# Performance work log

Hardware: AMD Instinct MI355X
Metric: run time of the kernel (lower is better)

Reference implementation:

```python
import jax, jax.numpy as jnp
import numpy as np

N, E, H = 20000, 640000, 128
EPS_BN = 1e-5
EPS_NORM = 1e-6


def batchnorm(x, gamma, beta):
    # BatchNorm1d in training mode: biased batch stats over dim 0
    mean = x.mean(axis=0)
    var = x.var(axis=0)
    return (x - mean) * jax.lax.rsqrt(var + EPS_BN) * gamma + beta


def setup_inputs() -> dict:
    key = jax.random.key(0)
    ks = jax.random.split(key, 10)
    s = 1.0 / np.sqrt(H)
    s3 = 1.0 / np.sqrt(3 * H)
    return {
        "edge_index": jax.random.randint(ks[0], (2, E), 0, N, dtype=jnp.int64),
        "node_features": jax.random.normal(ks[1], (N, H), dtype=jnp.float32),
        "edge_features": jax.random.normal(ks[2], (E, H), dtype=jnp.float32),
        "Wg": jax.random.uniform(ks[3], (H, 3 * H), jnp.float32, -s3, s3),
        "bg": jax.random.uniform(ks[4], (H,), jnp.float32, -s3, s3),
        "Ws": jax.random.uniform(ks[5], (H, H), jnp.float32, -s, s),
        "bs": jax.random.uniform(ks[6], (H,), jnp.float32, -s, s),
        "Wd": jax.random.uniform(ks[7], (H, H), jnp.float32, -s, s),
        "bd": jax.random.uniform(ks[8], (H,), jnp.float32, -s, s),
        "z_gamma": jnp.ones((H,), jnp.float32),
        "z_beta": jnp.zeros((H,), jnp.float32),
        "n_gamma": jnp.ones((H,), jnp.float32),
        "n_beta": jnp.zeros((H,), jnp.float32),
    }


def reference(edge_index, node_features, edge_features, Wg, bg, Ws, bs, Wd, bd,
              z_gamma, z_beta, n_gamma, n_beta):
    src = edge_index[0]
    dst = edge_index[1]
    n_nodes = node_features.shape[0]

    # edge gate: gather-concat-linear-BN-SiLU
    z = jnp.concatenate([node_features[src], node_features[dst], edge_features], axis=1)  # [E,3H]
    updated_edge = jax.nn.silu(batchnorm(z @ Wg.T + bg, z_gamma, z_beta))  # [E,H]

    # normalize edges: sigmoid, scatter-sum by src, gather back, divide
    sig = jax.nn.sigmoid(updated_edge)
    agg = jax.ops.segment_sum(sig, src, num_segments=n_nodes)  # [N,H]
    normalized = sig / (agg[src] + EPS_NORM)  # [E,H]

    # aggregate nodes: linear-gather-scale-scatter + linear
    upd_src = node_features @ Ws.T + bs  # [N,H]
    thee = (node_features @ Wd.T + bd)[dst]  # [E,H]
    upd_dst = jax.ops.segment_sum(normalized * thee, src, num_segments=n_nodes)  # [N,H]
    h = upd_src + upd_dst

    updated_nodes = node_features + jax.nn.silu(batchnorm(h, n_gamma, n_beta))
    return updated_nodes, updated_edge
```

## Files before the change

kernel.cpp:

```cpp
#include <hip/hip_runtime.h>
#include <cstddef>

#define DEVINL __device__ __forceinline__

typedef __attribute__((ext_vector_type(8))) short bf16x8;
typedef __attribute__((ext_vector_type(4))) float f32x4;

DEVINL unsigned short f2bf(float f) {
  unsigned int u = __builtin_bit_cast(unsigned int, f);
  u += 0x7FFFu + ((u >> 16) & 1u);
  return (unsigned short)(u >> 16);
}

DEVINL float sigm(float x) { return 1.0f / (1.0f + __expf(-x)); }

__global__ __launch_bounds__(256) void node_gemm_k(
    const float* __restrict__ nf, const float* __restrict__ Wg,
    const float* __restrict__ Ws, const float* __restrict__ bs,
    const float* __restrict__ Wd, const float* __restrict__ bd,
    float* __restrict__ A, float* __restrict__ Bm,
    float* __restrict__ S, float* __restrict__ D, int N) {
  __shared__ float sNf[32 * 128];
  const int n0 = blockIdx.x * 32;
  for (int i = threadIdx.x; i < 1024; i += 256) {
    const int r = i >> 5, k = (i & 31) << 2;
    float4 v = make_float4(0.f, 0.f, 0.f, 0.f);
    if (n0 + r < N) v = *(const float4*)(nf + (size_t)(n0 + r) * 128 + k);
    *(float4*)(&sNf[r * 128 + k]) = v;
  }
  __syncthreads();
  const int c = threadIdx.x & 127, g = threadIdx.x >> 7;
  const float4* w0p = (const float4*)(Wg + (size_t)c * 384);
  const float4* w1p = (const float4*)(Wg + (size_t)c * 384 + 128);
  const float4* w2p = (const float4*)(Ws + (size_t)c * 128);
  const float4* w3p = (const float4*)(Wd + (size_t)c * 128);
  float a0[16], a1[16], a2[16], a3[16];
#pragma unroll
  for (int n = 0; n < 16; ++n) { a0[n] = 0.f; a1[n] = 0.f; a2[n] = 0.f; a3[n] = 0.f; }
#pragma unroll 4
  for (int k4 = 0; k4 < 32; ++k4) {
    const float4 w0 = w0p[k4], w1 = w1p[k4], w2 = w2p[k4], w3 = w3p[k4];
#pragma unroll
    for (int n = 0; n < 16; ++n) {
      const float4 x = *(const float4*)(&sNf[(g * 16 + n) * 128 + (k4 << 2)]);
      a0[n] += x.x * w0.x + x.y * w0.y + x.z * w0.z + x.w * w0.w;
      a1[n] += x.x * w1.x + x.y * w1.y + x.z * w1.z + x.w * w1.w;
      a2[n] += x.x * w2.x + x.y * w2.y + x.z * w2.z + x.w * w2.w;
      a3[n] += x.x * w3.x + x.y * w3.y + x.z * w3.z + x.w * w3.w;
    }
  }
  const float bsv = bs[c], bdv = bd[c];
#pragma unroll
  for (int n = 0; n < 16; ++n) {
    const int node = n0 + g * 16 + n;
    if (node < N) {
      const size_t o = (size_t)node * 128 + c;
      A[o] = a0[n];
      Bm[o] = a1[n];
      S[o] = a2[n] + bsv;
      D[o] = a3[n] + bdv;
    }
  }
}

__global__ __launch_bounds__(256) void hist_k(const int* __restrict__ src,
                                              int* __restrict__ cnt, int E) {
  const int stride = gridDim.x * 256;
  for (int e = blockIdx.x * 256 + threadIdx.x; e < E; e += stride)
    atomicAdd(&cnt[src[e]], 1);
}

__global__ __launch_bounds__(1024) void scan_k(const int* __restrict__ cnt,
                                               int* __restrict__ off,
                                               int* __restrict__ cur, int N) {
  __shared__ int s[1024];
  const int tid = threadIdx.x;
  const int per = (N + 1023) >> 10;
  const int base = tid * per;
  int mysum = 0;
  for (int j = 0; j < per; ++j) {
    const int i = base + j;
    if (i < N) mysum += cnt[i];
  }
  s[tid] = mysum;
  __syncthreads();
  for (int d = 1; d < 1024; d <<= 1) {
    int v = 0;
    if (tid >= d) v = s[tid - d];
    __syncthreads();
    s[tid] += v;
    __syncthreads();
  }
  int run = s[tid] - mysum;
  for (int j = 0; j < per; ++j) {
    const int i = base + j;
    if (i < N) { off[i] = run; cur[i] = run; run += cnt[i]; }
  }
  if (tid == 1023) off[N] = s[1023];
}

__global__ __launch_bounds__(256) void scatter_k(const int* __restrict__ src,
                                                 int* __restrict__ cur,
                                                 int* __restrict__ list, int E) {
  const int stride = gridDim.x * 256;
  for (int e = blockIdx.x * 256 + threadIdx.x; e < E; e += stride) {
    const int p = atomicAdd(&cur[src[e]], 1);
    list[p] = e;
  }
}

__global__ __launch_bounds__(256, 4) void edge_lin_k(
    const int* __restrict__ ei, const float* __restrict__ ef,
    const float* __restrict__ Wg,
    const float* __restrict__ A, const float* __restrict__ Bm,
    float* __restrict__ lin, float* __restrict__ esum, float* __restrict__ esq,
    int E, int numTiles) {
  __shared__ __align__(16) short sW[128 * 136];

  const int tid = threadIdx.x;
  const int lane = tid & 63, wv = tid >> 6;
  const int l15 = lane & 15, quad = lane >> 4;
  const int r0 = wv << 4;
  const int* __restrict__ srcI = ei;
  const int* __restrict__ dstI = ei + E;

  for (int i = tid; i < 4096; i += 256) {
    const int c = i >> 5, k = (i & 31) << 2;
    const float4 v = *(const float4*)(Wg + (size_t)c * 384 + 256 + k);
    *(short4*)(&sW[c * 136 + k]) = make_short4((short)f2bf(v.x), (short)f2bf(v.y),
                                               (short)f2bf(v.z), (short)f2bf(v.w));
  }
  __syncthreads();

  float sAc[8], qAc[8];
#pragma unroll
  for (int t = 0; t < 8; ++t) { sAc[t] = 0.f; qAc[t] = 0.f; }

  for (int tile = blockIdx.x; tile < numTiles; tile += gridDim.x) {
    const int e0 = tile << 6;
    const int er = e0 + r0 + l15;
    const bool rvalid = (er < E);
    const float* __restrict__ efr = ef + (size_t)er * 128 + quad * 8;
    bf16x8 afr[4];
#pragma unroll
    for (int k0 = 0; k0 < 4; ++k0) {
      float4 u = make_float4(0.f, 0.f, 0.f, 0.f), v = make_float4(0.f, 0.f, 0.f, 0.f);
      if (rvalid) {
        u = *(const float4*)(efr + k0 * 32);
        v = *(const float4*)(efr + k0 * 32 + 4);
      }
      bf16x8 a;
      a[0] = (short)f2bf(u.x); a[1] = (short)f2bf(u.y);
      a[2] = (short)f2bf(u.z); a[3] = (short)f2bf(u.w);
      a[4] = (short)f2bf(v.x); a[5] = (short)f2bf(v.y);
      a[6] = (short)f2bf(v.z); a[7] = (short)f2bf(v.w);
      afr[k0] = a;
    }

    f32x4 acc[8];
#pragma unroll
    for (int t = 0; t < 8; ++t) acc[t] = (f32x4){0.f, 0.f, 0.f, 0.f};
#pragma unroll
    for (int k0 = 0; k0 < 4; ++k0) {
#pragma unroll
      for (int t = 0; t < 8; ++t) {
        const bf16x8 b = *(const bf16x8*)(&sW[(t * 16 + l15) * 136 + k0 * 32 + quad * 8]);
        acc[t] = __builtin_amdgcn_mfma_f32_16x16x32_bf16(afr[k0], b, acc[t], 0, 0, 0);
      }
    }

#pragma unroll
    for (int i = 0; i < 4; ++i) {
      const int rl = r0 + quad * 4 + i;
      const int e = e0 + rl;
      if (e < E) {
        const int sN = srcI[e], dN = dstI[e];
        const float* __restrict__ Ar = A + (size_t)sN * 128;
        const float* __restrict__ Br = Bm + (size_t)dN * 128;
        float* __restrict__ Lr = lin + (size_t)e * 128;
#pragma unroll
        for (int t = 0; t < 8; ++t) {
          const int c = t * 16 + l15;
          const float l = acc[t][i] + Ar[c] + Br[c];
          Lr[c] = l;
          sAc[t] += l;
          qAc[t] += l * l;
        }
      }
    }
  }

  __syncthreads();
  float* red = (float*)sW;
#pragma unroll
  for (int t = 0; t < 8; ++t) {
    float s = sAc[t], q = qAc[t];
    s += __shfl_xor(s, 16); s += __shfl_xor(s, 32);
    q += __shfl_xor(q, 16); q += __shfl_xor(q, 32);
    if (quad == 0) {
      red[wv * 128 + t * 16 + l15] = s;
      red[512 + wv * 128 + t * 16 + l15] = q;
    }
  }
  __syncthreads();
  if (tid < 128) {
    const float s = red[tid] + red[128 + tid] + red[256 + tid] + red[384 + tid];
    const float q = red[512 + tid] + red[640 + tid] + red[768 + tid] + red[896 + tid];
    unsafeAtomicAdd(&esum[tid], s);
    unsafeAtomicAdd(&esq[tid], q);
  }
}

__global__ __launch_bounds__(128) void finalize_bn_k(
    const float* __restrict__ sum, const float* __restrict__ sq,
    const float* __restrict__ gamma, const float* __restrict__ beta,
    float inv_cnt, float* __restrict__ scale, float* __restrict__ shift) {
  const int c = threadIdx.x;
  const float mean = sum[c] * inv_cnt;
  const float var = sq[c] * inv_cnt - mean * mean;
  const float sc = gamma[c] * rsqrtf(var + 1e-5f);
  scale[c] = sc;
  shift[c] = beta[c] - mean * sc;
}

__global__ __launch_bounds__(256) void node_agg_k(
    float* __restrict__ ue,
    const int* __restrict__ list, const int* __restrict__ off,
    const int* __restrict__ dstI, const float* __restrict__ D,
    const float* __restrict__ S,
    const float* __restrict__ scE, const float* __restrict__ shE,
    float* __restrict__ hvec, float* __restrict__ nsum, float* __restrict__ nsq,
    int N) {
  const int tid = threadIdx.x;
  const int lane = tid & 63, wv = tid >> 6;
  const int c0 = lane << 1;
  const int nw = gridDim.x << 2;
  const float2 sc = *(const float2*)(scE + c0);
  const float2 sh = *(const float2*)(shE + c0);
  float psx = 0.f, psy = 0.f, pqx = 0.f, pqy = 0.f;

  for (int n = (blockIdx.x << 2) + wv; n < N; n += nw) {
    const int o0 = off[n], o1 = off[n + 1];
    float agx = 0.f, agy = 0.f, tcx = 0.f, tcy = 0.f;
    for (int i = o0; i < o1; ++i) {
      const int e = list[i];
      const int d = dstI[e];
      const float2 u = *(const float2*)(ue + (size_t)e * 128 + c0);
      const float2 g = *(const float2*)(D + (size_t)d * 128 + c0);
      const float yx = u.x * sc.x + sh.x;
      const float yy = u.y * sc.y + sh.y;
      const float uex = yx * sigm(yx);
      const float uey = yy * sigm(yy);
      *(float2*)(ue + (size_t)e * 128 + c0) = make_float2(uex, uey);
      const float sgx = sigm(uex), sgy = sigm(uey);
      agx += sgx; agy += sgy;
      tcx += sgx * g.x; tcy += sgy * g.y;
    }
    const float2 sv = *(const float2*)(S + (size_t)n * 128 + c0);
    const float hx = sv.x + tcx / (agx + 1e-6f);
    const float hy = sv.y + tcy / (agy + 1e-6f);
    *(float2*)(hvec + (size_t)n * 128 + c0) = make_float2(hx, hy);
    psx += hx; psy += hy;
    pqx += hx * hx; pqy += hy * hy;
  }

  __shared__ float red[1024];
  red[wv * 128 + c0] = psx;
  red[wv * 128 + c0 + 1] = psy;
  red[512 + wv * 128 + c0] = pqx;
  red[512 + wv * 128 + c0 + 1] = pqy;
  __syncthreads();
  if (tid < 128) {
    const float s = red[tid] + red[128 + tid] + red[256 + tid] + red[384 + tid];
    const float q = red[512 + tid] + red[640 + tid] + red[768 + tid] + red[896 + tid];
    unsafeAtomicAdd(&nsum[tid], s);
    unsafeAtomicAdd(&nsq[tid], q);
  }
}

__global__ __launch_bounds__(256) void node_out_k(
    const float* __restrict__ nf, const float* __restrict__ hvec,
    const float* __restrict__ scale, const float* __restrict__ shift,
    float* __restrict__ out, int total) {
  const int stride = gridDim.x * 256;
  for (int idx = blockIdx.x * 256 + threadIdx.x; idx < total; idx += stride) {
    const int h = idx & 127;
    const float y = hvec[idx] * scale[h] + shift[h];
    out[idx] = nf[idx] + y * sigm(y);
  }
}

extern "C" void kernel_launch(void* const* d_in, const int* in_sizes, int n_in,
                              void* d_out, int out_size, void* d_ws, size_t ws_size,
                              hipStream_t stream) {
  const int* ei = (const int*)d_in[0];
  const float* nf = (const float*)d_in[1];
  const float* ef = (const float*)d_in[2];
  const float* Wg = (const float*)d_in[3];
  const float* Ws = (const float*)d_in[5];
  const float* bs = (const float*)d_in[6];
  const float* Wd = (const float*)d_in[7];
  const float* bd = (const float*)d_in[8];
  const float* zg = (const float*)d_in[9];
  const float* zb = (const float*)d_in[10];
  const float* ng = (const float*)d_in[11];
  const float* nb = (const float*)d_in[12];

  const int N = in_sizes[1] / 128;
  const int E = in_sizes[2] / 128;
  const size_t NH = (size_t)N * 128;

  float* ws = (float*)d_ws;
  float* A    = ws;
  float* Bm   = A + NH;
  float* S    = Bm + NH;
  float* D    = S + NH;
  float* hvec = D + NH;
  float* st   = hvec + NH;
  float* esum = st;
  float* esq  = st + 128;
  float* nsum = st + 256;
  float* nsq  = st + 384;
  float* scE  = st + 512;
  float* shE  = st + 640;
  float* scN  = st + 768;
  float* shN  = st + 896;
  int* cnt  = (int*)(st + 1024);
  int* off  = cnt + N;
  int* cur  = off + N + 1;
  int* list = cur + N;

  float* outN = (float*)d_out;
  float* outE = outN + NH;

  hipMemsetAsync(st, 0, (size_t)(1024 + N) * sizeof(float), stream);

  node_gemm_k<<<(N + 31) / 32, 256, 0, stream>>>(nf, Wg, Ws, bs, Wd, bd, A, Bm, S, D, N);

  hist_k<<<640, 256, 0, stream>>>(ei, cnt, E);
  scan_k<<<1, 1024, 0, stream>>>(cnt, off, cur, N);
  scatter_k<<<640, 256, 0, stream>>>(ei, cur, list, E);

  const int numTiles = (E + 63) / 64;
  const int gblocks = numTiles < 1024 ? numTiles : 1024;
  edge_lin_k<<<gblocks, 256, 0, stream>>>(ei, ef, Wg, A, Bm, outE, esum, esq, E, numTiles);
  finalize_bn_k<<<1, 128, 0, stream>>>(esum, esq, zg, zb, 1.0f / (float)E, scE, shE);

  node_agg_k<<<(N + 3) / 4, 256, 0, stream>>>(outE, list, off, ei + E, D, S, scE, shE,
                                              hvec, nsum, nsq, N);
  finalize_bn_k<<<1, 128, 0, stream>>>(nsum, nsq, ng, nb, 1.0f / (float)N, scN, shN);
  node_out_k<<<640, 256, 0, stream>>>(nf, hvec, scN, shN, outN, (int)NH);
}
```

Measured before the change: 1.222 ms.

## Store intermediates in fp16, fuse BN finalize into consumers, add nontemporal accesses

Stores the per-node projections A, B and D in fp16. Stores the pre-BN edge linear output in an fp16 workspace buffer when there is room, and reads it back in the aggregation kernel. The two finalize_bn launches are removed by computing scale and shift per block in shared memory, and streaming loads and stores are marked nontemporal. The aim is to cut gather and writeback bandwidth on the large E×H tensors, at some precision cost in the intermediates.

```diff
diff --git a/kernel.cpp b/kernel.cpp
--- a/kernel.cpp
+++ b/kernel.cpp
@@ -3,8 +3,11 @@
 
 #define DEVINL __device__ __forceinline__
 
+typedef _Float16 f16;
+typedef __attribute__((ext_vector_type(2))) _Float16 f16x2;
 typedef __attribute__((ext_vector_type(8))) short bf16x8;
 typedef __attribute__((ext_vector_type(4))) float f32x4;
+typedef __attribute__((ext_vector_type(2))) float f32x2;
 
 DEVINL unsigned short f2bf(float f) {
   unsigned int u = __builtin_bit_cast(unsigned int, f);
@@ -18,8 +21,8 @@
     const float* __restrict__ nf, const float* __restrict__ Wg,
     const float* __restrict__ Ws, const float* __restrict__ bs,
     const float* __restrict__ Wd, const float* __restrict__ bd,
-    float* __restrict__ A, float* __restrict__ Bm,
-    float* __restrict__ S, float* __restrict__ D, int N) {
+    f16* __restrict__ Ah, f16* __restrict__ Bh,
+    float* __restrict__ S, f16* __restrict__ Dh, int N) {
   __shared__ float sNf[32 * 128];
   const int n0 = blockIdx.x * 32;
   for (int i = threadIdx.x; i < 1024; i += 256) {
@@ -55,10 +58,10 @@
     const int node = n0 + g * 16 + n;
     if (node < N) {
       const size_t o = (size_t)node * 128 + c;
-      A[o] = a0[n];
-      Bm[o] = a1[n];
+      Ah[o] = (f16)a0[n];
+      Bh[o] = (f16)a1[n];
       S[o] = a2[n] + bsv;
-      D[o] = a3[n] + bdv;
+      Dh[o] = (f16)(a3[n] + bdv);
     }
   }
 }
@@ -109,11 +112,13 @@
   }
 }
 
+template <bool L16>
 __global__ __launch_bounds__(256, 4) void edge_lin_k(
     const int* __restrict__ ei, const float* __restrict__ ef,
     const float* __restrict__ Wg,
-    const float* __restrict__ A, const float* __restrict__ Bm,
-    float* __restrict__ lin, float* __restrict__ esum, float* __restrict__ esq,
+    const f16* __restrict__ Ah, const f16* __restrict__ Bh,
+    f16* __restrict__ linh, float* __restrict__ linf,
+    float* __restrict__ esum, float* __restrict__ esq,
     int E, int numTiles) {
   __shared__ __align__(16) short sW[128 * 136];
 
@@ -144,16 +149,16 @@
     bf16x8 afr[4];
 #pragma unroll
     for (int k0 = 0; k0 < 4; ++k0) {
-      float4 u = make_float4(0.f, 0.f, 0.f, 0.f), v = make_float4(0.f, 0.f, 0.f, 0.f);
+      f32x4 u = (f32x4){0.f, 0.f, 0.f, 0.f}, v = (f32x4){0.f, 0.f, 0.f, 0.f};
       if (rvalid) {
-        u = *(const float4*)(efr + k0 * 32);
-        v = *(const float4*)(efr + k0 * 32 + 4);
+        u = __builtin_nontemporal_load((const f32x4*)(efr + k0 * 32));
+        v = __builtin_nontemporal_load((const f32x4*)(efr + k0 * 32 + 4));
       }
       bf16x8 a;
-      a[0] = (short)f2bf(u.x); a[1] = (short)f2bf(u.y);
-      a[2] = (short)f2bf(u.z); a[3] = (short)f2bf(u.w);
-      a[4] = (short)f2bf(v.x); a[5] = (short)f2bf(v.y);
-      a[6] = (short)f2bf(v.z); a[7] = (short)f2bf(v.w);
+      a[0] = (short)f2bf(u[0]); a[1] = (short)f2bf(u[1]);
+      a[2] = (short)f2bf(u[2]); a[3] = (short)f2bf(u[3]);
+      a[4] = (short)f2bf(v[0]); a[5] = (short)f2bf(v[1]);
+      a[6] = (short)f2bf(v[2]); a[7] = (short)f2bf(v[3]);
       afr[k0] = a;
     }
 
@@ -175,14 +180,17 @@
       const int e = e0 + rl;
       if (e < E) {
         const int sN = srcI[e], dN = dstI[e];
-        const float* __restrict__ Ar = A + (size_t)sN * 128;
-        const float* __restrict__ Br = Bm + (size_t)dN * 128;
-        float* __restrict__ Lr = lin + (size_t)e * 128;
+        const f16* __restrict__ Ar = Ah + (size_t)sN * 128;
+        const f16* __restrict__ Br = Bh + (size_t)dN * 128;
 #pragma unroll
         for (int t = 0; t < 8; ++t) {
           const int c = t * 16 + l15;
-          const float l = acc[t][i] + Ar[c] + Br[c];
-          Lr[c] = l;
+          const float l = acc[t][i] + (float)Ar[c] + (float)Br[c];
+          if (L16) {
+            __builtin_nontemporal_store((f16)l, linh + (size_t)e * 128 + c);
+          } else {
+            __builtin_nontemporal_store(l, linf + (size_t)e * 128 + c);
+          }
           sAc[t] += l;
           qAc[t] += l * l;
         }
@@ -211,55 +219,62 @@
   }
 }
 
-__global__ __launch_bounds__(128) void finalize_bn_k(
-    const float* __restrict__ sum, const float* __restrict__ sq,
-    const float* __restrict__ gamma, const float* __restrict__ beta,
-    float inv_cnt, float* __restrict__ scale, float* __restrict__ shift) {
-  const int c = threadIdx.x;
-  const float mean = sum[c] * inv_cnt;
-  const float var = sq[c] * inv_cnt - mean * mean;
-  const float sc = gamma[c] * rsqrtf(var + 1e-5f);
-  scale[c] = sc;
-  shift[c] = beta[c] - mean * sc;
-}
-
+template <bool L16>
 __global__ __launch_bounds__(256) void node_agg_k(
-    float* __restrict__ ue,
+    const f16* __restrict__ linh, float* __restrict__ outE,
     const int* __restrict__ list, const int* __restrict__ off,
-    const int* __restrict__ dstI, const float* __restrict__ D,
+    const int* __restrict__ dstI, const f16* __restrict__ Dh,
     const float* __restrict__ S,
-    const float* __restrict__ scE, const float* __restrict__ shE,
+    const float* __restrict__ esum, const float* __restrict__ esq,
+    const float* __restrict__ zg, const float* __restrict__ zb, float invE,
     float* __restrict__ hvec, float* __restrict__ nsum, float* __restrict__ nsq,
     int N) {
+  __shared__ float sSc[128], sSh[128];
   const int tid = threadIdx.x;
+  if (tid < 128) {
+    const float mean = esum[tid] * invE;
+    const float var = esq[tid] * invE - mean * mean;
+    const float sc = zg[tid] * rsqrtf(var + 1e-5f);
+    sSc[tid] = sc;
+    sSh[tid] = zb[tid] - mean * sc;
+  }
+  __syncthreads();
+
   const int lane = tid & 63, wv = tid >> 6;
   const int c0 = lane << 1;
   const int nw = gridDim.x << 2;
-  const float2 sc = *(const float2*)(scE + c0);
-  const float2 sh = *(const float2*)(shE + c0);
+  const float scx = sSc[c0], scy = sSc[c0 + 1];
+  const float shx = sSh[c0], shy = sSh[c0 + 1];
   float psx = 0.f, psy = 0.f, pqx = 0.f, pqy = 0.f;
 
   for (int n = (blockIdx.x << 2) + wv; n < N; n += nw) {
     const int o0 = off[n], o1 = off[n + 1];
     float agx = 0.f, agy = 0.f, tcx = 0.f, tcy = 0.f;
+    int e = 0, d = 0;
+    if (o0 < o1) { e = list[o0]; d = dstI[e]; }
     for (int i = o0; i < o1; ++i) {
-      const int e = list[i];
-      const int d = dstI[e];
-      const float2 u = *(const float2*)(ue + (size_t)e * 128 + c0);
-      const float2 g = *(const float2*)(D + (size_t)d * 128 + c0);
-      const float yx = u.x * sc.x + sh.x;
-      const float yy = u.y * sc.y + sh.y;
-      const float uex = yx * sigm(yx);
-      const float uey = yy * sigm(yy);
-      *(float2*)(ue + (size_t)e * 128 + c0) = make_float2(uex, uey);
+      float lx, ly;
+      if (L16) {
+        const f16x2 u = __builtin_nontemporal_load((const f16x2*)(linh + (size_t)e * 128 + c0));
+        lx = (float)u.x; ly = (float)u.y;
+      } else {
+        const f32x2 u = __builtin_nontemporal_load((const f32x2*)(outE + (size_t)e * 128 + c0));
+        lx = u.x; ly = u.y;
+      }
+      const f16x2 g = *(const f16x2*)(Dh + (size_t)d * 128 + c0);
+      const int ec = e;
+      if (i + 1 < o1) { e = list[i + 1]; d = dstI[e]; }
+      const float yx = lx * scx + shx, yy = ly * scy + shy;
+      const float uex = yx * sigm(yx), uey = yy * sigm(yy);
+      __builtin_nontemporal_store((f32x2){uex, uey}, (f32x2*)(outE + (size_t)ec * 128 + c0));
       const float sgx = sigm(uex), sgy = sigm(uey);
       agx += sgx; agy += sgy;
-      tcx += sgx * g.x; tcy += sgy * g.y;
-    }
-    const float2 sv = *(const float2*)(S + (size_t)n * 128 + c0);
+      tcx += sgx * (float)g.x; tcy += sgy * (float)g.y;
+    }
+    const f32x2 sv = *(const f32x2*)(S + (size_t)n * 128 + c0);
     const float hx = sv.x + tcx / (agx + 1e-6f);
     const float hy = sv.y + tcy / (agy + 1e-6f);
-    *(float2*)(hvec + (size_t)n * 128 + c0) = make_float2(hx, hy);
+    __builtin_nontemporal_store((f32x2){hx, hy}, (f32x2*)(hvec + (size_t)n * 128 + c0));
     psx += hx; psy += hy;
     pqx += hx * hx; pqy += hy * hy;
   }
@@ -280,13 +295,25 @@
 
 __global__ __launch_bounds__(256) void node_out_k(
     const float* __restrict__ nf, const float* __restrict__ hvec,
-    const float* __restrict__ scale, const float* __restrict__ shift,
+    const float* __restrict__ nsum, const float* __restrict__ nsq,
+    const float* __restrict__ ng, const float* __restrict__ nb, float invN,
     float* __restrict__ out, int total) {
+  __shared__ float sSc[128], sSh[128];
+  if (threadIdx.x < 128) {
+    const int c = threadIdx.x;
+    const float mean = nsum[c] * invN;
+    const float var = nsq[c] * invN - mean * mean;
+    const float sc = ng[c] * rsqrtf(var + 1e-5f);
+    sSc[c] = sc;
+    sSh[c] = nb[c] - mean * sc;
+  }
+  __syncthreads();
   const int stride = gridDim.x * 256;
   for (int idx = blockIdx.x * 256 + threadIdx.x; idx < total; idx += stride) {
     const int h = idx & 127;
-    const float y = hvec[idx] * scale[h] + shift[h];
-    out[idx] = nf[idx] + y * sigm(y);
+    const float y = __builtin_nontemporal_load(hvec + idx) * sSc[h] + sSh[h];
+    const float o = __builtin_nontemporal_load(nf + idx) + y * sigm(y);
+    __builtin_nontemporal_store(o, out + idx);
   }
 }
 
@@ -310,32 +337,36 @@
   const int E = in_sizes[2] / 128;
   const size_t NH = (size_t)N * 128;
 
-  float* ws = (float*)d_ws;
-  float* A    = ws;
-  float* Bm   = A + NH;
-  float* S    = Bm + NH;
-  float* D    = S + NH;
-  float* hvec = D + NH;
-  float* st   = hvec + NH;
+  char* p = (char*)d_ws;
+  auto alloc = [&](size_t bytes) {
+    char* r = p;
+    p += (bytes + 255) & ~(size_t)255;
+    return r;
+  };
+  float* S    = (float*)alloc(NH * 4);
+  float* hvec = (float*)alloc(NH * 4);
+  f16* Ah = (f16*)alloc(NH * 2);
+  f16* Bh = (f16*)alloc(NH * 2);
+  f16* Dh = (f16*)alloc(NH * 2);
+  float* st = (float*)alloc(1024 * 4);
   float* esum = st;
   float* esq  = st + 128;
   float* nsum = st + 256;
   float* nsq  = st + 384;
-  float* scE  = st + 512;
-  float* shE  = st + 640;
-  float* scN  = st + 768;
-  float* shN  = st + 896;
-  int* cnt  = (int*)(st + 1024);
-  int* off  = cnt + N;
-  int* cur  = off + N + 1;
-  int* list = cur + N;
+  int* cnt  = (int*)alloc((size_t)N * 4);
+  int* off  = (int*)alloc((size_t)(N + 1) * 4);
+  int* cur  = (int*)alloc((size_t)N * 4);
+  int* list = (int*)alloc((size_t)E * 4);
+  f16* linh = (f16*)p;
+  const bool L16 =
+      ((size_t)(p - (char*)d_ws) + (size_t)E * 128 * 2) <= ws_size;
 
   float* outN = (float*)d_out;
   float* outE = outN + NH;
 
-  hipMemsetAsync(st, 0, (size_t)(1024 + N) * sizeof(float), stream);
-
-  node_gemm_k<<<(N + 31) / 32, 256, 0, stream>>>(nf, Wg, Ws, bs, Wd, bd, A, Bm, S, D, N);
+  hipMemsetAsync(st, 0, (size_t)((char*)cnt + (size_t)N * 4 - (char*)st), stream);
+
+  node_gemm_k<<<(N + 31) / 32, 256, 0, stream>>>(nf, Wg, Ws, bs, Wd, bd, Ah, Bh, S, Dh, N);
 
   hist_k<<<640, 256, 0, stream>>>(ei, cnt, E);
   scan_k<<<1, 1024, 0, stream>>>(cnt, off, cur, N);
@@ -343,11 +374,19 @@
 
   const int numTiles = (E + 63) / 64;
   const int gblocks = numTiles < 1024 ? numTiles : 1024;
-  edge_lin_k<<<gblocks, 256, 0, stream>>>(ei, ef, Wg, A, Bm, outE, esum, esq, E, numTiles);
-  finalize_bn_k<<<1, 128, 0, stream>>>(esum, esq, zg, zb, 1.0f / (float)E, scE, shE);
-
-  node_agg_k<<<(N + 3) / 4, 256, 0, stream>>>(outE, list, off, ei + E, D, S, scE, shE,
-                                              hvec, nsum, nsq, N);
-  finalize_bn_k<<<1, 128, 0, stream>>>(nsum, nsq, ng, nb, 1.0f / (float)N, scN, shN);
-  node_out_k<<<640, 256, 0, stream>>>(nf, hvec, scN, shN, outN, (int)NH);
-}
+  if (L16) {
+    edge_lin_k<true><<<gblocks, 256, 0, stream>>>(ei, ef, Wg, Ah, Bh, linh, nullptr,
+                                                  esum, esq, E, numTiles);
+    node_agg_k<true><<<(N + 3) / 4, 256, 0, stream>>>(
+        linh, outE, list, off, ei + E, Dh, S, esum, esq, zg, zb, 1.0f / (float)E,
+        hvec, nsum, nsq, N);
+  } else {
+    edge_lin_k<false><<<gblocks, 256, 0, stream>>>(ei, ef, Wg, Ah, Bh, nullptr, outE,
+                                                   esum, esq, E, numTiles);
+    node_agg_k<false><<<(N + 3) / 4, 256, 0, stream>>>(
+        nullptr, outE, list, off, ei + E, Dh, S, esum, esq, zg, zb, 1.0f / (float)E,
+        hvec, nsum, nsq, N);
+  }
+  node_out_k<<<640, 256, 0, stream>>>(nf, hvec, nsum, nsq, ng, nb, 1.0f / (float)N,
+                                      outN, (int)NH);
+}
```

After: 1.160 ms. 5.1% less time.
